# Kernel tuning notes

Hardware: AMD Instinct MI355X
Metric: run time of the kernel (lower is better)

Reference implementation:

```python
import jax, jax.numpy as jnp
import numpy as np

T_KD = 20.0      # KL_divergence temperature
T_THR = 6.0      # Threshold_weights temperature
EPS = 1e-05


def _margin(o, gathered):
    # torch.sort descending, take top-2; margin only when target is the argmax value
    top2 = jax.lax.top_k(o, 2)[0]                      # [B, 2]
    return jnp.where(top2[:, 0] == gathered, top2[:, 0] - top2[:, 1], 0.0)


def _forward(outputs1, outputs2, outputs3, outputs4, out_s, targets):
    B = targets.shape[0]
    idx = jnp.arange(B)
    mimic = (outputs1 + outputs2 + outputs3 + outputs4) / 4.0

    teachers = [outputs1, outputs2, outputs3, outputs4, mimic]
    gathered = [t[idx, targets] for t in teachers]      # each [B]

    # C = min over gathered target logits of the 4 real teachers
    C = jnp.minimum(jnp.minimum(gathered[0].min(), gathered[1].min()),
                    jnp.minimum(gathered[2].min(), gathered[3].min()))
    # if C < 0: shift everything by (-C + eps); else no shift
    shift = jnp.where(C < 0, -C + EPS, 0.0)

    shifted = [t + shift for t in teachers]
    g_shift = [g + shift for g in gathered]

    # Threshold_weights: margin per branch, softmax over 5 branches
    preds = jnp.stack([_margin(s, g) for s, g in zip(shifted, g_shift)], axis=1)  # [B,5]
    out_threshold = jax.nn.softmax(preds / T_THR, axis=1)

    # max over the 4 (shifted) teacher logit tensors
    max_preds = jnp.maximum(jnp.maximum(shifted[0].max(), shifted[1].max()),
                            jnp.maximum(shifted[2].max(), shifted[3].max()))

    # per-sample CE of student (shared across branches)
    log_p_s = jax.nn.log_softmax(out_s, axis=1)
    CE = -log_p_s[idx, targets]                          # [B]

    log_ps_T = jax.nn.log_softmax(out_s / T_KD, axis=1)  # [B,C]

    def branch_loss(teacher, g_s):
        w2 = g_s / max_preds          # weights2
        w1 = 1.0 - w2                 # weights1
        log_pt = jax.nn.log_softmax(teacher / T_KD, axis=1)
        p_t = jnp.exp(log_pt)
        KD = jnp.sum(p_t * (log_pt - log_ps_T), axis=1) * (T_KD * T_KD)  # [B]
        return w1 * CE + w2 * KD

    # KD/CE use the ORIGINAL (unshifted) teacher logits
    losses = jnp.stack([branch_loss(t, g) for t, g in zip(teachers, g_shift)], axis=1)  # [B,5]
    return jnp.mean(jnp.sum(out_threshold * losses, axis=1))


def setup_inputs() -> dict:
    key = jax.random.key(0)
    ks = jax.random.split(key, 6)
    B, C = 8192, 1000
    return {
        "outputs1": jax.random.normal(ks[0], (B, C), dtype=jnp.float32),
        "outputs2": jax.random.normal(ks[1], (B, C), dtype=jnp.float32),
        "outputs3": jax.random.normal(ks[2], (B, C), dtype=jnp.float32),
        "outputs4": jax.random.normal(ks[3], (B, C), dtype=jnp.float32),
        "out_s": jax.random.normal(ks[4], (B, C), dtype=jnp.float32),
        "targets": jax.random.randint(ks[5], (B,), 0, C, dtype=jnp.int64 if jax.config.jax_enable_x64 else jnp.int32),
    }


def reference(outputs1, outputs2, outputs3, outputs4, out_s, targets):
    return _forward(outputs1, outputs2, outputs3, outputs4, out_s, targets)
```

## Files before the change

### kernel.cpp

```cpp
#include <hip/hip_runtime.h>
#include <math.h>

#define NB 8192
#define NC 1000
#define NF4 250


#define LOG2E 1.4426950408889634f
#define LN2   0.6931471805599453f

__device__ __forceinline__ float fexp2(float x) { return __builtin_amdgcn_exp2f(x); }
__device__ __forceinline__ float flog2(float x) { return __builtin_amdgcn_logf(x); }

#define VMWAIT(N)                                        \
  asm volatile("s_waitcnt vmcnt(" #N ")" ::: "memory");  \
  __builtin_amdgcn_sched_barrier(0)
#define LGKM0                                            \
  asm volatile("s_waitcnt lgkmcnt(0)" ::: "memory");     \
  __builtin_amdgcn_sched_barrier(0)

typedef const __attribute__((address_space(1))) unsigned int gu32;
typedef __attribute__((address_space(3))) unsigned int lu32;
__device__ __forceinline__ void stage16(const void* g, void* l) {
  __builtin_amdgcn_global_load_lds((gu32*)g, (lu32*)l, 16, 0, 0);
}

template <int CTRL>
__device__ __forceinline__ float dpp_mov(float v, float ident) {
  return __uint_as_float((unsigned)__builtin_amdgcn_update_dpp(
      (int)__float_as_uint(ident), (int)__float_as_uint(v), CTRL, 0xF, 0xF,
      false));
}

__device__ __forceinline__ float dppredsum(float v) {
  v += dpp_mov<0x111>(v, 0.f);
  v += dpp_mov<0x112>(v, 0.f);
  v += dpp_mov<0x114>(v, 0.f);
  v += dpp_mov<0x118>(v, 0.f);
  v += dpp_mov<0x142>(v, 0.f);
  v += dpp_mov<0x143>(v, 0.f);
  return v;
}

__device__ __forceinline__ void dppredtop2(float& t1, float& t2) {
  const float NI = -INFINITY;
#define T2STEP(C)                                   \
  {                                                 \
    float i1 = dpp_mov<C>(t1, NI);                  \
    float i2 = dpp_mov<C>(t2, NI);                  \
    t2 = fmaxf(fmaxf(t2, i2), fminf(t1, i1));       \
    t1 = fmaxf(t1, i1);                             \
  }
  T2STEP(0x111) T2STEP(0x112) T2STEP(0x114) T2STEP(0x118)
  T2STEP(0x142) T2STEP(0x143)
#undef T2STEP
}

__device__ __forceinline__ float wredsum(float v) {
#pragma unroll
  for (int m = 32; m >= 1; m >>= 1) v += __shfl_xor(v, m, 64);
  return v;
}
__device__ __forceinline__ float wredmax(float v) {
#pragma unroll
  for (int m = 32; m >= 1; m >>= 1) v = fmaxf(v, __shfl_xor(v, m, 64));
  return v;
}
__device__ __forceinline__ float wredmin(float v) {
#pragma unroll
  for (int m = 32; m >= 1; m >>= 1) v = fminf(v, __shfl_xor(v, m, 64));
  return v;
}
__device__ __forceinline__ float f4get(const float4& v, int e) {
  return e == 0 ? v.x : e == 1 ? v.y : e == 2 ? v.z : v.w;
}

__device__ __forceinline__ void proc_chunk(
    const float4& c1, const float4& c2, const float4& c3, const float4& c4,
    const float4& cs, float t1[5], float t2[5], float Z[5], float S1[5],
    float& Z1, float& Z20) {
  const float K20 = LOG2E / 20.0f;
#pragma unroll
  for (int e = 0; e < 4; ++e) {
    float w0 = f4get(c1, e);
    float w1 = f4get(c2, e);
    float w2 = f4get(c3, e);
    float w3 = f4get(c4, e);
    float wsv = f4get(cs, e);
    float wm = ((w0 + w1) + w2 + w3) * 0.25f;
    float w[5] = {w0, w1, w2, w3, wm};
#pragma unroll
    for (int t = 0; t < 5; ++t) {
      t2[t] = fmaxf(t2[t], fminf(t1[t], w[t]));
      t1[t] = fmaxf(t1[t], w[t]);
      float et = fexp2(w[t] * K20);
      Z[t] += et;
      S1[t] = fmaf(et, w[t] - wsv, S1[t]);
    }
    Z1 += fexp2(wsv * LOG2E);
    Z20 += fexp2(wsv * K20);
  }
}

__global__ __launch_bounds__(256, 4) void k_rowstats(
    const float* __restrict__ o1, const float* __restrict__ o2,
    const float* __restrict__ o3, const float* __restrict__ o4,
    const float* __restrict__ os, const int* __restrict__ tg,
    float* __restrict__ ws, float* __restrict__ out) {
  const int lane = threadIdx.x & 63;
  const int wv = threadIdx.x >> 6;
  const int row = (blockIdx.x << 2) + wv;
  const size_t base = (size_t)row * NC;

  __shared__ float4 lds[4][2][5][64];

  if (blockIdx.x == 0 && threadIdx.x == 0) out[0] = 0.0f;

  const int target = tg[row];
  const float g1 = o1[base + target];
  const float g2 = o2[base + target];
  const float g3 = o3[base + target];
  const float g4 = o4[base + target];
  const float gs = os[base + target];

#define STAGE(i, b)                                                       \
  do {                                                                    \
    int f_ = lane + ((i) << 6);                                           \
    if (f_ > NF4 - 1) f_ = NF4 - 1;    \
    stage16((const float4*)(o1 + base) + f_, &lds[wv][b][0][0]);          \
    stage16((const float4*)(o2 + base) + f_, &lds[wv][b][1][0]);          \
    stage16((const float4*)(o3 + base) + f_, &lds[wv][b][2][0]);          \
    stage16((const float4*)(o4 + base) + f_, &lds[wv][b][3][0]);          \
    stage16((const float4*)(os + base) + f_, &lds[wv][b][4][0]);          \
  } while (0)

  STAGE(0, 0);
  STAGE(1, 1);

  float t1[5], t2[5], Z[5], S1[5];
#pragma unroll
  for (int t = 0; t < 5; ++t) {
    t1[t] = -INFINITY; t2[t] = -INFINITY; Z[t] = 0.f; S1[t] = 0.f;
  }
  float Z1 = 0.f, Z20 = 0.f;
  float4 r1, r2, r3, r4, rs;

#define READC(b)                                                          \
  r1 = lds[wv][b][0][lane]; r2 = lds[wv][b][1][lane];                     \
  r3 = lds[wv][b][2][lane]; r4 = lds[wv][b][3][lane];                     \
  rs = lds[wv][b][4][lane];

  VMWAIT(5);
  READC(0);
  LGKM0;
  STAGE(2, 0);
  proc_chunk(r1, r2, r3, r4, rs, t1, t2, Z, S1, Z1, Z20);

  VMWAIT(5);
  READC(1);
  LGKM0;
  STAGE(3, 1);
  proc_chunk(r1, r2, r3, r4, rs, t1, t2, Z, S1, Z1, Z20);

  VMWAIT(5);
  READC(0);
  LGKM0;
  proc_chunk(r1, r2, r3, r4, rs, t1, t2, Z, S1, Z1, Z20);

  VMWAIT(0);
  READC(1);
  LGKM0;
  if (lane < 58)
    proc_chunk(r1, r2, r3, r4, rs, t1, t2, Z, S1, Z1, Z20);

#pragma unroll
  for (int t = 0; t < 5; ++t) dppredtop2(t1[t], t2[t]);
#pragma unroll
  for (int t = 0; t < 5; ++t) { Z[t] = dppredsum(Z[t]); S1[t] = dppredsum(S1[t]); }
  Z1 = dppredsum(Z1);
  Z20 = dppredsum(Z20);

  if (lane == 63) {
    const float gm = ((g1 + g2) + g3 + g4) * 0.25f;
    float gg[5] = {g1, g2, g3, g4, gm};

    const float lse_s = flog2(Z20) * LN2;
    const float CE = flog2(Z1) * LN2 - gs;

#pragma unroll
    for (int t = 0; t < 5; ++t) {
      float lse_t = flog2(Z[t]) * LN2;
      float KD = 400.0f * (S1[t] / (20.0f * Z[t]) - lse_t + lse_s);
      float margin = (t1[t] == gg[t]) ? (t1[t] - t2[t]) : 0.0f;
      ws[(size_t)t * NB + row] = margin;
      ws[(size_t)(5 + t) * NB + row] = gg[t];
      ws[(size_t)(10 + t) * NB + row] = KD;
    }
    ws[(size_t)15 * NB + row] = CE;
    ws[(size_t)16 * NB + row] = fminf(fminf(g1, g2), fminf(g3, g4));
    ws[(size_t)17 * NB + row] = fmaxf(fmaxf(t1[0], t1[1]), fmaxf(t1[2], t1[3]));
  }
#undef STAGE
#undef READC
}

__global__ __launch_bounds__(64) void k_final(const float* __restrict__ ws,
                                              float* __restrict__ out) {
  const int lane = threadIdx.x;

  float mn = INFINITY, mx = -INFINITY;
  const float4* mnp = (const float4*)(ws + (size_t)16 * NB);
  const float4* mxp = (const float4*)(ws + (size_t)17 * NB);
#pragma unroll
  for (int k = 0; k < 32; ++k) {
    int r4 = lane + (k << 6);
    float4 a = mnp[r4];
    float4 b = mxp[r4];
    mn = fminf(mn, fminf(fminf(a.x, a.y), fminf(a.z, a.w)));
    mx = fmaxf(mx, fmaxf(fmaxf(b.x, b.y), fmaxf(b.z, b.w)));
  }
  mn = wredmin(mn);
  mx = wredmax(mx);
  const float shift = (mn < 0.0f) ? (-mn + 1e-5f) : 0.0f;
  const float maxp = mx + shift;

  const int r = blockIdx.x * 64 + lane;
  const float K6 = LOG2E / 6.0f;

  float m[5], e[5];
#pragma unroll
  for (int t = 0; t < 5; ++t) m[t] = ws[(size_t)t * NB + r];
  float pm = fmaxf(fmaxf(fmaxf(m[0], m[1]), fmaxf(m[2], m[3])), m[4]);
  float Zl = 0.0f;
#pragma unroll
  for (int t = 0; t < 5; ++t) { e[t] = fexp2((m[t] - pm) * K6); Zl += e[t]; }
  float ce = ws[(size_t)15 * NB + r];
  float rl = 0.0f;
#pragma unroll
  for (int t = 0; t < 5; ++t) {
    float g = ws[(size_t)(5 + t) * NB + r];
    float kd = ws[(size_t)(10 + t) * NB + r];
    float w2 = (g + shift) / maxp;
    float loss = (1.0f - w2) * ce + w2 * kd;
    rl += e[t] * loss;
  }
  float acc = wredsum(rl / Zl);
  if (lane == 0) atomicAdd(out, acc * (1.0f / 8192.0f));
}

extern "C" void kernel_launch(void* const* d_in, const int* in_sizes, int n_in,
                              void* d_out, int out_size, void* d_ws, size_t ws_size,
                              hipStream_t stream) {
  const float* o1 = (const float*)d_in[0];
  const float* o2 = (const float*)d_in[1];
  const float* o3 = (const float*)d_in[2];
  const float* o4 = (const float*)d_in[3];
  const float* os = (const float*)d_in[4];
  const int* tg = (const int*)d_in[5];
  float* ws = (float*)d_ws;
  float* out = (float*)d_out;

  k_rowstats<<<NB / 4, 256, 0, stream>>>(o1, o2, o3, o4, os, tg, ws, out);
  k_final<<<NB / 64, 64, 0, stream>>>(ws, out);
}
```

Baseline: 187.7 us.

## Single-buffer LDS staging and raise occupancy target in rowstats kernel

Replaces the per-wave double-buffered LDS staging with a single buffer, halving shared memory per block. The launch-bounds minimum blocks per multiprocessor goes from 4 to 8, so more waves are resident to hide memory latency. In exchange, each chunk now waits for its own load to fully complete before the next load is issued, which serializes load and compute within a wave. The tighter launch bound may also limit registers.

```diff
diff --git a/kernel.cpp b/kernel.cpp
--- a/kernel.cpp
+++ b/kernel.cpp
@@ -102,7 +102,7 @@
   }
 }
 
-__global__ __launch_bounds__(256, 4) void k_rowstats(
+__global__ __launch_bounds__(256, 8) void k_rowstats(
     const float* __restrict__ o1, const float* __restrict__ o2,
     const float* __restrict__ o3, const float* __restrict__ o4,
     const float* __restrict__ os, const int* __restrict__ tg,
@@ -112,7 +112,7 @@
   const int row = (blockIdx.x << 2) + wv;
   const size_t base = (size_t)row * NC;
 
-  __shared__ float4 lds[4][2][5][64];
+  __shared__ float4 lds[4][5][64];
 
   if (blockIdx.x == 0 && threadIdx.x == 0) out[0] = 0.0f;
 
@@ -123,19 +123,18 @@
   const float g4 = o4[base + target];
   const float gs = os[base + target];
 
-#define STAGE(i, b)                                                       \
+#define STAGE(i)                                                          \
   do {                                                                    \
     int f_ = lane + ((i) << 6);                                           \
     if (f_ > NF4 - 1) f_ = NF4 - 1;    \
-    stage16((const float4*)(o1 + base) + f_, &lds[wv][b][0][0]);          \
-    stage16((const float4*)(o2 + base) + f_, &lds[wv][b][1][0]);          \
-    stage16((const float4*)(o3 + base) + f_, &lds[wv][b][2][0]);          \
-    stage16((const float4*)(o4 + base) + f_, &lds[wv][b][3][0]);          \
-    stage16((const float4*)(os + base) + f_, &lds[wv][b][4][0]);          \
+    stage16((const float4*)(o1 + base) + f_, &lds[wv][0][0]);             \
+    stage16((const float4*)(o2 + base) + f_, &lds[wv][1][0]);             \
+    stage16((const float4*)(o3 + base) + f_, &lds[wv][2][0]);             \
+    stage16((const float4*)(o4 + base) + f_, &lds[wv][3][0]);             \
+    stage16((const float4*)(os + base) + f_, &lds[wv][4][0]);             \
   } while (0)
 
-  STAGE(0, 0);
-  STAGE(1, 1);
+  STAGE(0);
 
   float t1[5], t2[5], Z[5], S1[5];
 #pragma unroll
@@ -145,30 +144,31 @@
   float Z1 = 0.f, Z20 = 0.f;
   float4 r1, r2, r3, r4, rs;
 
-#define READC(b)                                                          \
-  r1 = lds[wv][b][0][lane]; r2 = lds[wv][b][1][lane];                     \
-  r3 = lds[wv][b][2][lane]; r4 = lds[wv][b][3][lane];                     \
-  rs = lds[wv][b][4][lane];
-
-  VMWAIT(5);
-  READC(0);
-  LGKM0;
-  STAGE(2, 0);
+#define READC                                                             \
+  r1 = lds[wv][0][lane]; r2 = lds[wv][1][lane];                           \
+  r3 = lds[wv][2][lane]; r4 = lds[wv][3][lane];                           \
+  rs = lds[wv][4][lane];
+
+  VMWAIT(0);
+  READC;
+  LGKM0;
+  STAGE(1);
   proc_chunk(r1, r2, r3, r4, rs, t1, t2, Z, S1, Z1, Z20);
 
-  VMWAIT(5);
-  READC(1);
-  LGKM0;
-  STAGE(3, 1);
+  VMWAIT(0);
+  READC;
+  LGKM0;
+  STAGE(2);
   proc_chunk(r1, r2, r3, r4, rs, t1, t2, Z, S1, Z1, Z20);
 
-  VMWAIT(5);
-  READC(0);
-  LGKM0;
+  VMWAIT(0);
+  READC;
+  LGKM0;
+  STAGE(3);
   proc_chunk(r1, r2, r3, r4, rs, t1, t2, Z, S1, Z1, Z20);
 
   VMWAIT(0);
-  READC(1);
+  READC;
   LGKM0;
   if (lane < 58)
     proc_chunk(r1, r2, r3, r4, rs, t1, t2, Z, S1, Z1, Z20);
```

After: 214.4 us. +14.2%, slower.
